# Optimization experiments

Hardware: AMD Instinct MI355X
Metric: run time of the kernel (lower is better)

## Reference

```python
import jax, jax.numpy as jnp
import numpy as np

H = 12        # num heads
D = 128       # head dim
HID = 1536    # hidden size
CHUNK = 12    # attention_chunk_size
PAST = 12     # attention_context_left - 1
FUT = 0       # attention_context_right
CTX = CHUNK + PAST + FUT  # 24
SOFTCAP = 50.0
Q_SCALE = D ** -0.5 / np.log(2.0)
K_SCALE = np.log(1.0 + np.e) / np.log(2.0)


def setup_inputs() -> dict:
    key = jax.random.key(0)
    ks = jax.random.split(key, 8)
    B, S = 4, 6000
    s = HID ** -0.5
    x = jax.random.normal(ks[0], (B, S, HID), jnp.float32)
    pos_emb = jax.random.normal(ks[1], (CTX, HID), jnp.float32)
    Wq = jax.random.normal(ks[2], (HID, HID), jnp.float32) * s
    Wk = jax.random.normal(ks[3], (HID, HID), jnp.float32) * s
    Wv = jax.random.normal(ks[4], (HID, HID), jnp.float32) * s
    Wrel = jax.random.normal(ks[5], (HID, HID), jnp.float32) * s
    Wpost = jax.random.normal(ks[6], (HID, HID), jnp.float32) * s
    per_dim_scale = jax.random.normal(ks[7], (D,), jnp.float32) * 0.1
    return dict(x=x, pos_emb=pos_emb, Wq=Wq, Wk=Wk, Wv=Wv, Wrel=Wrel,
                Wpost=Wpost, per_dim_scale=per_dim_scale)


def _rel_shift(x):
    # Transformer-XL relative shift trick: pad last dim to CTX+1, flatten, crop.
    B, Hh, NB, BS, PL = x.shape
    x = jnp.pad(x, ((0, 0), (0, 0), (0, 0), (0, 0), (0, CTX + 1 - PL)))
    x = x.reshape(B, Hh, NB, BS * (CTX + 1))[..., :BS * CTX]
    return x.reshape(B, Hh, NB, BS, CTX)


def reference(x, pos_emb, Wq, Wk, Wv, Wrel, Wpost, per_dim_scale):
    B, S, _ = x.shape
    NB = (S + CHUNK - 1) // CHUNK
    pad = NB * CHUNK - S

    q = (x @ Wq.T).reshape(B, S, H, D) * (Q_SCALE * jax.nn.softplus(per_dim_scale))
    k = (x @ Wk.T).reshape(B, S, H, D) * K_SCALE
    v = (x @ Wv.T).reshape(B, S, H, D)

    # chunk queries: [B, NB, CHUNK, H, D]
    q_blocks = jnp.pad(q, ((0, 0), (0, pad), (0, 0), (0, 0))).reshape(B, NB, CHUNK, H, D)

    # block-local context windows (torch unfold equivalent): [B, NB, CTX, H, D]
    idx = (jnp.arange(NB) * CHUNK)[:, None] + jnp.arange(CTX)[None, :]

    def ctx_blocks(t):
        t = jnp.pad(t, ((0, 0), (PAST, FUT + CHUNK - 1), (0, 0), (0, 0)))
        return t[:, idx]

    k_ctx = ctx_blocks(k)
    v_ctx = ctx_blocks(v)

    rel_k = (pos_emb @ Wrel.T).reshape(-1, H, D)  # [PL, H, D]

    # content-content term: [B, H, NB, CHUNK, CTX]
    ac = jnp.einsum('bnqhd,bnkhd->bhnqk', q_blocks, k_ctx)
    # content-position term, then rel-shift
    bd = jnp.einsum('bnqhd,phd->bhnqp', q_blocks, rel_k)
    bd = _rel_shift(bd)

    logits = jnp.tanh((ac + bd) / SOFTCAP) * SOFTCAP

    # blocked local mask (True = attend); FUT == 0 so only past window.
    qi = (jnp.arange(NB) * CHUNK)[:, None, None] + jnp.arange(CHUNK)[None, :, None]
    kj = (jnp.arange(NB) * CHUNK)[:, None, None] + jnp.arange(CTX)[None, None, :] - PAST
    dist = qi - kj
    mask = (dist >= 0) & (dist < PAST) & (kj >= 0) & (kj < S) & (qi < S)

    logits = jnp.where(mask[None, None], logits, -1e9)
    attn = jax.nn.softmax(logits, axis=-1)

    out = jnp.einsum('bhnqk,bnkhd->bnqhd', attn, v_ctx)
    out = out.reshape(B, NB * CHUNK, H * D)[:, :S]
    return out @ Wpost.T
```

## Files before the change

### kernel.cpp

```cpp
#include <hip/hip_runtime.h>
#include <hip/hip_bf16.h>

#define BATCH 4
#define SEQ   6000
#define NHEAD 12
#define HDIM  128
#define HID   1536
#define CHUNK 12
#define CTXW  24
#define NBLK  500
#define MROWS (BATCH * SEQ)

#define Q_SCALE_D (0.08838834764831845 / 0.6931471805599453)
#define K_SCALE_D (1.3132616875182228 / 0.6931471805599453)

typedef __bf16 bf16x8 __attribute__((ext_vector_type(8)));
typedef float  floatx4 __attribute__((ext_vector_type(4)));

#define SAN_LIM 1e15f
__device__ __forceinline__ float san(float f) {
    return fminf(fmaxf(f, -SAN_LIM), SAN_LIM);
}

__device__ __forceinline__ void gload16(const void* g, void* l) {
    __builtin_amdgcn_global_load_lds(
        (__attribute__((address_space(1))) void*)g,
        (__attribute__((address_space(3))) void*)l,
        16, 0, 0);
}

__global__ void qscale_kernel(const float* __restrict__ pds,
                              float* __restrict__ qs) {
    int d = threadIdx.x;
    float x = san(pds[d]);
    float sp = (x > 20.0f) ? x : log1pf(expf(x));
    qs[d] = san((float)Q_SCALE_D * sp);
}

__device__ __forceinline__ void cvt4(const float* __restrict__ src,
                                     __hip_bfloat16* __restrict__ dst, int i) {
    float4 f = ((const float4*)src)[i];
    union { __hip_bfloat16 h[4]; uint2 u; } cv;
    cv.h[0] = __float2bfloat16(san(f.x));
    cv.h[1] = __float2bfloat16(san(f.y));
    cv.h[2] = __float2bfloat16(san(f.z));
    cv.h[3] = __float2bfloat16(san(f.w));
    ((uint2*)dst)[i] = cv.u;
}

__global__ void convert_x_kernel(const float* __restrict__ src,
                                 __hip_bfloat16* __restrict__ dst, int n4) {
    int stride = gridDim.x * blockDim.x;
    for (int i = blockIdx.x * blockDim.x + threadIdx.x; i < n4; i += stride)
        cvt4(src, dst, i);
}

__global__ void convert_misc_kernel(
    const float* __restrict__ Wq, const float* __restrict__ Wk,
    const float* __restrict__ Wv, const float* __restrict__ Wrel,
    const float* __restrict__ Wpost, const float* __restrict__ pos,
    __hip_bfloat16* __restrict__ Wqkv, __hip_bfloat16* __restrict__ Wrelb,
    __hip_bfloat16* __restrict__ Wpostb, __hip_bfloat16* __restrict__ posb) {
    const float* src;
    __hip_bfloat16* dst;
    int n4 = 589824;
    switch (blockIdx.y) {
        case 0: src = Wq;    dst = Wqkv;            break;
        case 1: src = Wk;    dst = Wqkv + 2359296;  break;
        case 2: src = Wv;    dst = Wqkv + 4718592;  break;
        case 3: src = Wrel;  dst = Wrelb;           break;
        case 4: src = Wpost; dst = Wpostb;          break;
        default: src = pos;  dst = posb; n4 = 9216; break;
    }
    int i = blockIdx.x * 256 + threadIdx.x;
    if (i < n4) cvt4(src, dst, i);
}

template<int QKV, int CDT>
__device__ __forceinline__ void gemm_bb_core(
    const __hip_bfloat16* __restrict__ A,
    const __hip_bfloat16* __restrict__ W,
    void* __restrict__ C0, void* __restrict__ C1, void* __restrict__ C2,
    int M, int K, const float* __restrict__ qscale)
{
    __shared__ __align__(16) __hip_bfloat16 As[128 * 32];
    __shared__ __align__(16) __hip_bfloat16 Bs[128 * 32];

    const int tid   = threadIdx.x;
    const int wave  = tid >> 6;
    const int lane  = tid & 63;
    const int tileM = blockIdx.y * 128;
    const int tileN = blockIdx.x * 128;

    const int sr = (wave << 4) + (lane >> 2);
    const int sc = (lane & 3) << 3;
    int ar0 = tileM + sr;      if (ar0 > M - 1) ar0 = M - 1;
    int ar1 = tileM + sr + 64; if (ar1 > M - 1) ar1 = M - 1;
    const __hip_bfloat16* ag0 = A + (size_t)ar0 * K + sc;
    const __hip_bfloat16* ag1 = A + (size_t)ar1 * K + sc;
    const __hip_bfloat16* bg0 = W + (size_t)(tileN + sr) * K + sc;
    const __hip_bfloat16* bg1 = W + (size_t)(tileN + sr + 64) * K + sc;
    __hip_bfloat16* la0 = As + (wave << 9);
    __hip_bfloat16* la1 = As + 2048 + (wave << 9);
    __hip_bfloat16* lb0 = Bs + (wave << 9);
    __hip_bfloat16* lb1 = Bs + 2048 + (wave << 9);

    const int wr   = (wave >> 1) << 6;
    const int wc   = (wave & 1) << 6;
    const int frow = lane & 15;
    const int fk   = (lane >> 4) << 3;

    floatx4 acc[4][4] = {};

    for (int k0 = 0; k0 < K; k0 += 32) {
        __syncthreads();
        gload16(ag0 + k0, la0);
        gload16(ag1 + k0, la1);
        gload16(bg0 + k0, lb0);
        gload16(bg1 + k0, lb1);
        __syncthreads();

        bf16x8 af[4], bfv[4];
        #pragma unroll
        for (int i = 0; i < 4; ++i)
            af[i] = *(const bf16x8*)&As[(wr + i * 16 + frow) * 32 + fk];
        #pragma unroll
        for (int j = 0; j < 4; ++j)
            bfv[j] = *(const bf16x8*)&Bs[(wc + j * 16 + frow) * 32 + fk];
        #pragma unroll
        for (int i = 0; i < 4; ++i)
            #pragma unroll
            for (int j = 0; j < 4; ++j)
                acc[i][j] = __builtin_amdgcn_mfma_f32_16x16x32_bf16(
                    af[i], bfv[j], acc[i][j], 0, 0, 0);
    }

    const int orow = (lane >> 4) << 2;
    if (QKV) {
        const int z = tileN / 1536;
        __hip_bfloat16* C =
            (__hip_bfloat16*)(z == 0 ? C0 : (z == 1 ? C1 : C2));
        const int cb = tileN - z * 1536 + wc;
        #pragma unroll
        for (int i = 0; i < 4; ++i) {
            #pragma unroll
            for (int r = 0; r < 4; ++r) {
                int row = tileM + wr + i * 16 + orow + r;
                if (row < M) {
                    #pragma unroll
                    for (int j = 0; j < 4; ++j) {
                        int col = cb + j * 16 + frow;
                        float v = acc[i][j][r];
                        if (z == 0)      v *= qscale[col & 127];
                        else if (z == 1) v *= (float)K_SCALE_D;
                        C[(size_t)row * HID + col] = __float2bfloat16(v);
                    }
                }
            }
        }
    } else {
        #pragma unroll
        for (int i = 0; i < 4; ++i) {
            #pragma unroll
            for (int r = 0; r < 4; ++r) {
                int row = tileM + wr + i * 16 + orow + r;
                if (row < M) {
                    #pragma unroll
                    for (int j = 0; j < 4; ++j) {
                        int col = tileN + wc + j * 16 + frow;
                        float v = acc[i][j][r];
                        if (CDT == 0)
                            ((__hip_bfloat16*)C0)[(size_t)row * HID + col] =
                                __float2bfloat16(v);
                        else
                            ((float*)C0)[(size_t)row * HID + col] = v;
                    }
                }
            }
        }
    }
}

__global__ __launch_bounds__(256, 2)
void gemm_qkv_bb(const __hip_bfloat16* __restrict__ A,
                 const __hip_bfloat16* __restrict__ W,
                 __hip_bfloat16* __restrict__ Q,
                 __hip_bfloat16* __restrict__ Kb,
                 __hip_bfloat16* __restrict__ V,
                 const float* __restrict__ qscale, int M) {
    gemm_bb_core<1, 0>(A, W, Q, Kb, V, M, HID, qscale);
}

__global__ __launch_bounds__(256, 2)
void gemm_rel(const __hip_bfloat16* __restrict__ A,
              const __hip_bfloat16* __restrict__ W,
              __hip_bfloat16* __restrict__ C, int M) {
    gemm_bb_core<0, 0>(A, W, C, C, C, M, HID, nullptr);
}

__global__ __launch_bounds__(256, 2)
void gemm_post(const __hip_bfloat16* __restrict__ A,
               const __hip_bfloat16* __restrict__ W,
               float* __restrict__ C, int M) {
    gemm_bb_core<0, 1>(A, W, C, C, C, M, HID, nullptr);
}

__global__ __launch_bounds__(256)
void attn_kernel(const __hip_bfloat16* __restrict__ Q,
                 const __hip_bfloat16* __restrict__ Kt,
                 const __hip_bfloat16* __restrict__ Vt,
                 const __hip_bfloat16* __restrict__ R,
                 __hip_bfloat16* __restrict__ O)
{
    const int tid = threadIdx.x;
    int idx = blockIdx.x;
    const int h = idx % NHEAD;  idx /= NHEAD;
    const int n = idx % NBLK;   idx /= NBLK;
    const int b = idx;

    __shared__ __align__(16) __hip_bfloat16 qs[CHUNK * HDIM];
    __shared__ __align__(16) __hip_bfloat16 ks[23 * HDIM];
    __shared__ __align__(16) __hip_bfloat16 vs[23 * HDIM];
    __shared__ __align__(16) __hip_bfloat16 rs[CHUNK * HDIM];
    __shared__ float lg[CHUNK][CHUNK];

    const size_t rowbase = (size_t)b * SEQ + (size_t)n * CHUNK;
    const int hoff = h * HDIM;

    #pragma unroll
    for (int it = 0; it < 3; ++it) {
        int i = it * 256 + tid;
        int row = i >> 6;
        int cu  = i & 63;
        ((unsigned int*)qs)[i] =
            *(const unsigned int*)(Q + (rowbase + row) * HID + hoff + cu * 2);
    }
    #pragma unroll
    for (int it = 0; it < 6; ++it) {
        int i = it * 256 + tid;
        if (i < 1472) {
            int row = i >> 6;
            int cu  = i & 63;
            int g = n * CHUNK + row - 11;
            unsigned int kval = 0u, vval = 0u;
            if (g >= 0) {
                size_t off = ((size_t)b * SEQ + g) * HID + hoff + cu * 2;
                kval = *(const unsigned int*)(Kt + off);
                vval = *(const unsigned int*)(Vt + off);
            }
            ((unsigned int*)ks)[i] = kval;
            ((unsigned int*)vs)[i] = vval;
        }
    }
    #pragma unroll
    for (int it = 0; it < 3; ++it) {
        int i = it * 256 + tid;
        int j  = i >> 6;
        int cu = i & 63;
        ((unsigned int*)rs)[i] =
            *(const unsigned int*)(R + (size_t)(12 - j) * HID + hoff + cu * 2);
    }
    __syncthreads();

    if (tid < CHUNK * CHUNK) {
        int q = tid / CHUNK, j = tid % CHUNK;
        bool valid = (n > 0) || (j <= q);
        float acc = 0.0f;
        if (valid) {
            int krow = q + 11 - j;
            const __hip_bfloat16* qp = qs + q * HDIM;
            const __hip_bfloat16* kp = ks + krow * HDIM;
            const __hip_bfloat16* rp = rs + j * HDIM;
            #pragma unroll 16
            for (int d = 0; d < HDIM; ++d)
                acc += __bfloat162float(qp[d]) *
                       (__bfloat162float(kp[d]) + __bfloat162float(rp[d]));
            acc = tanhf(acc * 0.02f) * 50.0f;
        }
        lg[q][j] = valid ? acc : -1e30f;
    }
    __syncthreads();

    if (tid < CHUNK) {
        float m = -1e30f;
        #pragma unroll
        for (int j = 0; j < CHUNK; ++j) m = fmaxf(m, lg[tid][j]);
        float e[CHUNK];
        float s = 0.0f;
        #pragma unroll
        for (int j = 0; j < CHUNK; ++j) { e[j] = expf(lg[tid][j] - m); s += e[j]; }
        float inv = 1.0f / s;
        #pragma unroll
        for (int j = 0; j < CHUNK; ++j) lg[tid][j] = e[j] * inv;
    }
    __syncthreads();

    #pragma unroll
    for (int it = 0; it < 6; ++it) {
        int i = it * 256 + tid;
        int q = i >> 7, d = i & 127;
        float acc = 0.0f;
        #pragma unroll
        for (int j = 0; j < CHUNK; ++j)
            acc += lg[q][j] * __bfloat162float(vs[(q + 11 - j) * HDIM + d]);
        O[(rowbase + q) * HID + hoff + d] = __float2bfloat16(san(acc));
    }
}

extern "C" void kernel_launch(void* const* d_in, const int* in_sizes, int n_in,
                              void* d_out, int out_size, void* d_ws, size_t ws_size,
                              hipStream_t stream) {
    const float* x     = (const float*)d_in[0];
    const float* pos   = (const float*)d_in[1];
    const float* Wq    = (const float*)d_in[2];
    const float* Wk    = (const float*)d_in[3];
    const float* Wv    = (const float*)d_in[4];
    const float* Wv_   = (const float*)d_in[4];
    const float* Wrel  = (const float*)d_in[5];
    const float* Wpost = (const float*)d_in[6];
    const float* pds   = (const float*)d_in[7];
    float* out = (float*)d_out;
    (void)Wv_;

    char* ws = (char*)d_ws;
    float* qscale          = (float*)ws;
    __hip_bfloat16* Rk     = (__hip_bfloat16*)(ws + 1024);
    __hip_bfloat16* posb   = (__hip_bfloat16*)(ws + 1024 + 73728);
    __hip_bfloat16* Wqkv   = (__hip_bfloat16*)(ws + 1024 + 2 * 73728);
    __hip_bfloat16* Wrelb  = Wqkv + (size_t)3 * 1536 * 1536;
    __hip_bfloat16* Wpostb = Wrelb + (size_t)1536 * 1536;
    __hip_bfloat16* Qb     = Wpostb + (size_t)1536 * 1536;
    const size_t fixed = 1024 + 2 * 73728 +
                         (size_t)5 * 1536 * 1536 * 2;
    const size_t qk_full = 2 * (size_t)MROWS * HID * 2;

    int phases;
    if      (ws_size >= fixed + qk_full)     phases = 1;
    else if (ws_size >= fixed + qk_full / 2) phases = 2;
    else                                     phases = 4;
    const int    Bp = BATCH / phases;
    const size_t Mp = (size_t)Bp * SEQ;
    __hip_bfloat16* Kb = Qb + Mp * HID;

    qscale_kernel<<<1, 128, 0, stream>>>(pds, qscale);
    convert_misc_kernel<<<dim3(2304, 6), 256, 0, stream>>>(
        Wq, Wk, Wv, Wrel, Wpost, pos, Wqkv, Wrelb, Wpostb, posb);
    gemm_rel<<<dim3(12, 1), 256, 0, stream>>>(posb, Wrelb, Rk, CTXW);

    for (int p = 0; p < phases; ++p) {
        __hip_bfloat16* Xb =
            (__hip_bfloat16*)((char*)d_out + p * Mp * HID * 4);
        __hip_bfloat16* Vb = Xb + Mp * HID;

        convert_x_kernel<<<2048, 256, 0, stream>>>(
            x + p * Mp * HID, Xb, (int)(Mp * HID / 4));
        gemm_qkv_bb<<<dim3(36, (unsigned)((Mp + 127) / 128)), 256, 0, stream>>>(
            Xb, Wqkv, Qb, Kb, Vb, qscale, (int)Mp);
        attn_kernel<<<Bp * NBLK * NHEAD, 256, 0, stream>>>(Qb, Kb, Vb, Rk, Qb);
        gemm_post<<<dim3(12, (unsigned)((Mp + 127) / 128)), 256, 0, stream>>>(
            Qb, Wpostb, out + p * Mp * HID, (int)Mp);
    }
}
```

Baseline: 1.101 ms.

## Swizzle GEMM workgroup order and vectorize attention LDS loads with XOR swizzle

Remaps GEMM workgroup IDs so consecutive blocks are spread across XCD-like groups of eight, aiming at better L2 locality for shared operand tiles. The attention kernel now loads Q/K/V/R with 16-byte global loads into XOR-swizzled shared buffers and reads them as 8-wide vectors in the QK dot product, reducing load instruction count and LDS bank conflicts. The PV stage processes two output elements per thread and stores packed bf16 pairs. This adds index arithmetic and depends on the swizzle being applied consistently on write and read.

After: 1.019 ms. 1.08x faster.

```diff
diff --git a/kernel.cpp b/kernel.cpp
--- a/kernel.cpp
+++ b/kernel.cpp
@@ -16,10 +16,15 @@
 
 typedef __bf16 bf16x8 __attribute__((ext_vector_type(8)));
 typedef float  floatx4 __attribute__((ext_vector_type(4)));
+typedef unsigned short u16x8 __attribute__((ext_vector_type(8)));
 
 #define SAN_LIM 1e15f
 __device__ __forceinline__ float san(float f) {
     return fminf(fmaxf(f, -SAN_LIM), SAN_LIM);
+}
+
+__device__ __forceinline__ float bf2f(unsigned short b) {
+    return __uint_as_float((unsigned)b << 16);
 }
 
 __device__ __forceinline__ void gload16(const void* g, void* l) {
@@ -89,8 +94,15 @@
     const int tid   = threadIdx.x;
     const int wave  = tid >> 6;
     const int lane  = tid & 63;
-    const int tileM = blockIdx.y * 128;
-    const int tileN = blockIdx.x * 128;
+
+    const int gx   = gridDim.x;
+    const int nwg  = gx * gridDim.y;
+    const int orig = blockIdx.y * gx + blockIdx.x;
+    int wgid = orig;
+    if ((nwg & 7) == 0)
+        wgid = (orig & 7) * (nwg >> 3) + (orig >> 3);
+    const int tileN = (wgid % gx) * 128;
+    const int tileM = (wgid / gx) * 128;
 
     const int sr = (wave << 4) + (lane >> 2);
     const int sc = (lane & 3) << 3;
@@ -205,6 +217,10 @@
     gemm_bb_core<0, 1>(A, W, C, C, C, M, HID, nullptr);
 }
 
+__device__ __forceinline__ int swz(int byte) {
+    return byte ^ (((byte >> 8) & 7) << 4);
+}
+
 __global__ __launch_bounds__(256)
 void attn_kernel(const __hip_bfloat16* __restrict__ Q,
                  const __hip_bfloat16* __restrict__ Kt,
@@ -218,63 +234,68 @@
     const int n = idx % NBLK;   idx /= NBLK;
     const int b = idx;
 
-    __shared__ __align__(16) __hip_bfloat16 qs[CHUNK * HDIM];
-    __shared__ __align__(16) __hip_bfloat16 ks[23 * HDIM];
-    __shared__ __align__(16) __hip_bfloat16 vs[23 * HDIM];
-    __shared__ __align__(16) __hip_bfloat16 rs[CHUNK * HDIM];
+    __shared__ __align__(16) char qs[CHUNK * 256];
+    __shared__ __align__(16) char ks[23 * 256];
+    __shared__ __align__(16) char vs[23 * 256];
+    __shared__ __align__(16) char rs[CHUNK * 256];
     __shared__ float lg[CHUNK][CHUNK];
 
     const size_t rowbase = (size_t)b * SEQ + (size_t)n * CHUNK;
     const int hoff = h * HDIM;
 
+    #pragma unroll
+    for (int it = 0; it < 2; ++it) {
+        int i = it * 256 + tid;
+        if (i < 384) {
+            if (i < 192) {
+                int row = i >> 4, c = i & 15;
+                uint4 v = *(const uint4*)(Q + (rowbase + row) * HID + hoff + c * 8);
+                *(uint4*)(qs + swz(row * 256 + c * 16)) = v;
+            } else {
+                int t = i - 192;
+                int j = t >> 4, c = t & 15;
+                uint4 v = *(const uint4*)(R + (size_t)(12 - j) * HID + hoff + c * 8);
+                *(uint4*)(rs + swz(j * 256 + c * 16)) = v;
+            }
+        }
+    }
     #pragma unroll
     for (int it = 0; it < 3; ++it) {
         int i = it * 256 + tid;
-        int row = i >> 6;
-        int cu  = i & 63;
-        ((unsigned int*)qs)[i] =
-            *(const unsigned int*)(Q + (rowbase + row) * HID + hoff + cu * 2);
-    }
-    #pragma unroll
-    for (int it = 0; it < 6; ++it) {
-        int i = it * 256 + tid;
-        if (i < 1472) {
-            int row = i >> 6;
-            int cu  = i & 63;
+        if (i < 736) {
+            int t = (i < 368) ? i : i - 368;
+            int row = t >> 4, c = t & 15;
             int g = n * CHUNK + row - 11;
-            unsigned int kval = 0u, vval = 0u;
+            uint4 v = make_uint4(0u, 0u, 0u, 0u);
             if (g >= 0) {
-                size_t off = ((size_t)b * SEQ + g) * HID + hoff + cu * 2;
-                kval = *(const unsigned int*)(Kt + off);
-                vval = *(const unsigned int*)(Vt + off);
-            }
-            ((unsigned int*)ks)[i] = kval;
-            ((unsigned int*)vs)[i] = vval;
-        }
-    }
-    #pragma unroll
-    for (int it = 0; it < 3; ++it) {
-        int i = it * 256 + tid;
-        int j  = i >> 6;
-        int cu = i & 63;
-        ((unsigned int*)rs)[i] =
-            *(const unsigned int*)(R + (size_t)(12 - j) * HID + hoff + cu * 2);
+                v = *(const uint4*)(Kt + 0 * (size_t)HID +
+                                    ((size_t)b * SEQ + g) * HID + hoff + c * 8);
+                if (i >= 368)
+                    v = *(const uint4*)(Vt + ((size_t)b * SEQ + g) * HID + hoff + c * 8);
+            }
+            if (i < 368)
+                *(uint4*)(ks + swz(row * 256 + c * 16)) = v;
+            else
+                *(uint4*)(vs + t * 16) = v;
+        }
     }
     __syncthreads();
 
     if (tid < CHUNK * CHUNK) {
-        int q = tid / CHUNK, j = tid % CHUNK;
+        int q = tid / CHUNK, j = tid - (tid / CHUNK) * CHUNK;
         bool valid = (n > 0) || (j <= q);
         float acc = 0.0f;
         if (valid) {
             int krow = q + 11 - j;
-            const __hip_bfloat16* qp = qs + q * HDIM;
-            const __hip_bfloat16* kp = ks + krow * HDIM;
-            const __hip_bfloat16* rp = rs + j * HDIM;
-            #pragma unroll 16
-            for (int d = 0; d < HDIM; ++d)
-                acc += __bfloat162float(qp[d]) *
-                       (__bfloat162float(kp[d]) + __bfloat162float(rp[d]));
+            #pragma unroll
+            for (int c = 0; c < 16; ++c) {
+                u16x8 qv = *(const u16x8*)(qs + swz(q * 256 + c * 16));
+                u16x8 kv = *(const u16x8*)(ks + swz(krow * 256 + c * 16));
+                u16x8 rv = *(const u16x8*)(rs + swz(j * 256 + c * 16));
+                #pragma unroll
+                for (int e = 0; e < 8; ++e)
+                    acc += bf2f(qv[e]) * (bf2f(kv[e]) + bf2f(rv[e]));
+            }
             acc = tanhf(acc * 0.02f) * 50.0f;
         }
         lg[q][j] = valid ? acc : -1e30f;
@@ -296,14 +317,21 @@
     __syncthreads();
 
     #pragma unroll
-    for (int it = 0; it < 6; ++it) {
+    for (int it = 0; it < 3; ++it) {
         int i = it * 256 + tid;
-        int q = i >> 7, d = i & 127;
-        float acc = 0.0f;
-        #pragma unroll
-        for (int j = 0; j < CHUNK; ++j)
-            acc += lg[q][j] * __bfloat162float(vs[(q + 11 - j) * HDIM + d]);
-        O[(rowbase + q) * HID + hoff + d] = __float2bfloat16(san(acc));
+        int q = i >> 6, dp = i & 63;
+        float a0 = 0.0f, a1 = 0.0f;
+        #pragma unroll
+        for (int j = 0; j < CHUNK; ++j) {
+            float p = lg[q][j];
+            unsigned vv = *(const unsigned*)(vs + (q + 11 - j) * 256 + dp * 4);
+            a0 += p * bf2f((unsigned short)(vv & 0xffffu));
+            a1 += p * bf2f((unsigned short)(vv >> 16));
+        }
+        union { __hip_bfloat16 h[2]; unsigned u; } pk;
+        pk.h[0] = __float2bfloat16(san(a0));
+        pk.h[1] = __float2bfloat16(san(a1));
+        *(unsigned*)(O + (rowbase + q) * HID + hoff + dp * 2) = pk.u;
     }
 }
 
@@ -315,12 +343,10 @@
     const float* Wq    = (const float*)d_in[2];
     const float* Wk    = (const float*)d_in[3];
     const float* Wv    = (const float*)d_in[4];
-    const float* Wv_   = (const float*)d_in[4];
     const float* Wrel  = (const float*)d_in[5];
     const float* Wpost = (const float*)d_in[6];
     const float* pds   = (const float*)d_in[7];
     float* out = (float*)d_out;
-    (void)Wv_;
 
     char* ws = (char*)d_ws;
     float* qscale          = (float*)ws;
```
